# Performance work log

Hardware: AMD Instinct MI355X
Metric: run time of the kernel (lower is better)

The kernel has to match this reference:

```python
import jax, jax.numpy as jnp
import numpy as np

# Fixed Grossberg constants (registered buffers in the torch module)
TAU = 0.8          # time constant
DECAY = 0.15       # passive decay A
B_CAP = 1.0        # excitatory cap B
C_FLOOR = 0.1      # inhibitory floor C
LAT_INHIB = 3.0    # lateral inhibition strength
DIV_SIGMA = 0.3    # divisive normalization sigma
ALPHA = 1.5        # excitatory gating alpha
BETA = 0.75        # inhibitory gating beta

BATCH = 32768
N = 17
T = 128
DT = 0.05


def _dynamics(state, W_pos, W_neg, feasibility, P):
    """Grossberg shunting ODE right-hand side. state: [B,17]."""
    # valences evaluated with environmental perturbation
    val_eval = state[:, 13:17] + P[:, 13:17]                       # [B,4]
    gate_exc = jax.nn.sigmoid(ALPHA * val_eval)                    # [B,4]
    gate_inh = jax.nn.sigmoid(-BETA * val_eval)                    # [B,4]
    ones9 = jnp.ones_like(state[:, :9])
    ones4 = jnp.ones_like(gate_exc)
    # gates expanded over nodes: only action nodes (9:13) gated
    ge_full = jnp.concatenate([ones9, gate_exc, ones4], axis=1)    # [B,17]
    gi_full = jnp.concatenate([ones9, gate_inh, ones4], axis=1)    # [B,17]
    # row-gating of W is equivalent to gating the matvec output
    exc = ge_full * jnp.einsum('bij,bj->bi', W_pos, state)         # [B,17]
    inh = gi_full * jnp.einsum('bij,bj->bi', W_neg, state)         # [B,17]
    E = jax.nn.relu(exc)
    I = jax.nn.relu(inh)
    # environmental drive routed through shunting terms for need nodes
    E_needs = E[:, :9] + jax.nn.relu(P[:, :9])
    I_needs = I[:, :9] + jax.nn.relu(-P[:, :9])
    # feasibility gates action excitation; selective lateral inhibition:
    # each action inhibited by the (divisively normalized) sum of OTHER actions
    acts = state[:, 9:13]
    other_sum = jnp.sum(acts, axis=1, keepdims=True) - acts
    lateral = LAT_INHIB * other_sum / (DIV_SIGMA + other_sum)
    E_acts = E[:, 9:13] * feasibility
    I_acts = I[:, 9:13] + lateral
    E_full = jnp.concatenate([E_needs, E_acts, E[:, 13:17]], axis=1)
    I_full = jnp.concatenate([I_needs, I_acts, I[:, 13:17]], axis=1)
    # direct additive perturbation only on valence nodes
    P_direct = jnp.concatenate([jnp.zeros_like(state[:, :13]), P[:, 13:17]], axis=1)
    return (-DECAY * state + (B_CAP - state) * E_full
            - (C_FLOOR + state) * I_full + P_direct) / TAU


def setup_inputs() -> dict:
    key = jax.random.key(0)
    k0, k1, k2, k3, k4 = jax.random.split(key, 5)
    state0 = jax.random.uniform(k0, (BATCH, N), dtype=jnp.float32)
    W_pos = 0.2 * jax.random.uniform(k1, (BATCH, N, N), dtype=jnp.float32)
    W_neg = 0.2 * jax.random.uniform(k2, (BATCH, N, N), dtype=jnp.float32)
    feasibility = jax.random.uniform(k3, (BATCH, 4), dtype=jnp.float32)
    perturbation = 0.1 * jax.random.normal(k4, (BATCH, N), dtype=jnp.float32)
    t_eval = jnp.arange(T, dtype=jnp.float32) * DT
    return {"state0": state0, "W_pos": W_pos, "W_neg": W_neg,
            "feasibility": feasibility, "perturbation": perturbation,
            "t_eval": t_eval}


def reference(state0, W_pos, W_neg, feasibility, perturbation, t_eval):
    dt = t_eval[1] - t_eval[0]
    n_steps = t_eval.shape[0] - 1  # static

    def step(s, _):
        ds = _dynamics(s, W_pos, W_neg, feasibility, perturbation)
        raw = s + dt * ds
        new = jnp.concatenate([
            jnp.clip(raw[:, 0:9], 0.0, 1.0),     # needs
            jnp.clip(raw[:, 9:13], 0.0, 1.0),    # actions
            jnp.clip(raw[:, 13:17], -1.0, 1.0),  # valences
        ], axis=1)
        return new, new

    _, traj = jax.lax.scan(step, state0, None, length=n_steps)
    return jnp.concatenate([state0[None], traj], axis=0)  # [T, B, 17]
```

## Files before the change

### kernel.cpp

```cpp
#include <hip/hip_runtime.h>
#include <stdint.h>


typedef _Float16 h2 __attribute__((ext_vector_type(2)));
typedef __fp16 h2raw __attribute__((ext_vector_type(2)));
typedef float f4a __attribute__((ext_vector_type(4), aligned(4)));

static constexpr int BATCH = 32768;
static constexpr int NN = 17;
static constexpr int TT = 128;

__device__ __forceinline__ uint32_t pk(float a, float b) {
    h2raw h = __builtin_amdgcn_cvt_pkrtz(a, b);
    return __builtin_bit_cast(uint32_t, h);
}
__device__ __forceinline__ float dot2(uint32_t a, uint32_t b, float c) {
    return __builtin_amdgcn_fdot2(__builtin_bit_cast(h2, a),
                                  __builtin_bit_cast(h2, b), c, false);
}
__device__ __forceinline__ float lo16(uint32_t u) {
    h2 h = __builtin_bit_cast(h2, u); return (float)h.x;
}
__device__ __forceinline__ float hi16(uint32_t u) {
    h2 h = __builtin_bit_cast(h2, u); return (float)h.y;
}
template <int K>
__device__ __forceinline__ uint32_t qswz(uint32_t v) {
    return (uint32_t)__builtin_amdgcn_ds_swizzle((int)v, (K << 5) | 0x1C);
}

__global__ __launch_bounds__(256, 2) void hotco_kernel(
    const float* __restrict__ state0,
    const float* __restrict__ Wpos,
    const float* __restrict__ Wneg,
    const float* __restrict__ feas,
    const float* __restrict__ P,
    const float* __restrict__ t_eval,
    float* __restrict__ out)
{
    const int tid = blockIdx.x * blockDim.x + threadIdx.x;
    const int lane4 = tid & 3;
    const int b = tid >> 2;
    if (b >= BATCH) return;

    const int base = (lane4 == 0) ? 0 : (4 * lane4 + 1);
    const int nrows = (lane4 == 0) ? 5 : 4;

    constexpr int pA[9] = {0, 2, 4, 5, 7, 9, 11, 13, 15};
    constexpr int pB[9] = {1, 3, -1, 6, 8, 10, 12, 14, 16};

    uint32_t w[5][9], wn[5][9];
    {
        const float* wpb = Wpos + (size_t)b * (NN * NN);
        const float* wnb = Wneg + (size_t)b * (NN * NN);
#pragma unroll
        for (int t = 0; t < 5; ++t) {
            if (t < nrows) {
                const float* rp = wpb + (base + t) * NN;
                const float* rn = wnb + (base + t) * NN;
#pragma unroll
                for (int c = 0; c < 9; ++c) {
                    float a2 = (pB[c] < 0) ? 0.f : rp[pB[c]];
                    float b2 = (pB[c] < 0) ? 0.f : rn[pB[c]];
                    w[t][c]  = pk(rp[pA[c]], a2);
                    wn[t][c] = pk(rn[pA[c]], b2);
                }
            } else {
#pragma unroll
                for (int c = 0; c < 9; ++c) { w[t][c] = 0u; wn[t][c] = 0u; }
            }
        }
    }

    float cA[5], cB[5], pdv[4];
#pragma unroll
    for (int t = 0; t < 5; ++t) { cA[t] = 0.f; cB[t] = 0.f; }
#pragma unroll
    for (int t = 0; t < 4; ++t) pdv[t] = 0.f;
    if (lane4 < 2) {
#pragma unroll
        for (int t = 0; t < 5; ++t) {
            if (t < nrows) {
                float pv = P[(size_t)b * NN + base + t];
                cA[t] = fmaxf(pv, 0.f);
                cB[t] = fmaxf(-pv, 0.f);
            }
        }
    } else if (lane4 == 2) {
#pragma unroll
        for (int t = 0; t < 4; ++t) {
            cA[t] = feas[(size_t)b * 4 + t];
            cB[t] = P[(size_t)b * NN + 13 + t];
        }
    } else {
#pragma unroll
        for (int t = 0; t < 4; ++t)
            pdv[t] = P[(size_t)b * NN + 13 + t];
    }

    uint32_t s2[9];
    {
        const float* sb = state0 + (size_t)b * NN;
        float st[17];
#pragma unroll
        for (int j = 0; j < NN; ++j) st[j] = sb[j];
        s2[0] = pk(st[0], st[1]);   s2[1] = pk(st[2], st[3]);
        s2[2] = pk(st[4], 0.f);     s2[3] = pk(st[5], st[6]);
        s2[4] = pk(st[7], st[8]);   s2[5] = pk(st[9], st[10]);
        s2[6] = pk(st[11], st[12]); s2[7] = pk(st[13], st[14]);
        s2[8] = pk(st[15], st[16]);
    }
    float sOwn[5];
#pragma unroll
    for (int t = 0; t < 5; ++t)
        sOwn[t] = (t < nrows) ? state0[(size_t)b * NN + base + t] : 0.f;

    const float lo = (lane4 == 3) ? -1.f : 0.f;
    const float dtv = t_eval[1] - t_eval[0];
    const float k1 = dtv * 1.25f;
    const float C  = -1.0820212806667226f;

    {
        float* op = out + (size_t)b * NN + base;
        f4a v0; v0.x = sOwn[0]; v0.y = sOwn[1]; v0.z = sOwn[2]; v0.w = sOwn[3];
        *(f4a*)op = v0;
        if (nrows == 5) op[4] = sOwn[4];
    }
    float* outp = out + (size_t)BATCH * NN + (size_t)b * NN + base;

#pragma unroll 1
    for (int st = 1; st < TT; ++st) {
        float E5[5], I5[5];
#pragma unroll
        for (int t = 0; t < 5; ++t) {
            float ae = 0.f, ai = 0.f;
#pragma unroll
            for (int c = 0; c < 9; ++c) {
                ae = dot2(w[t][c], s2[c], ae);
                ai = dot2(wn[t][c], s2[c], ai);
            }
            E5[t] = fmaxf(ae, 0.f);
            I5[t] = fmaxf(ai, 0.f);
        }

        if (lane4 == 2) {
            const float sum_acts = sOwn[0] + sOwn[1] + sOwn[2] + sOwn[3];
            const float v13[4] = { lo16(s2[7]), hi16(s2[7]), lo16(s2[8]), hi16(s2[8]) };
#pragma unroll
            for (int t = 0; t < 4; ++t) {
                float v  = v13[t] + cB[t];
                float e1 = __builtin_amdgcn_exp2f(C * v);
                float ge = __builtin_amdgcn_rcpf(fmaf(e1, e1, 1.f));
                float gi = e1 * __builtin_amdgcn_rcpf(1.f + e1);
                E5[t] = ge * E5[t] * cA[t];
                float os  = sum_acts - sOwn[t];
                float lat = fmaf(-0.9f, __builtin_amdgcn_rcpf(0.3f + os), 3.0f);
                I5[t] = fmaf(gi, I5[t], lat);
            }
            E5[4] = 0.f; I5[4] = 0.f;
        } else {
#pragma unroll
            for (int t = 0; t < 5; ++t) { E5[t] += cA[t]; I5[t] += cB[t]; }
        }

#pragma unroll
        for (int t = 0; t < 5; ++t) {
            float s  = sOwn[t];
            float d0 = fmaf(-0.15f, s, (t < 4) ? pdv[t] : 0.f);
            float d1 = fmaf(1.f - s, E5[t], d0);
            float d2 = fmaf(-(0.1f + s), I5[t], d1);
            float raw = fmaf(k1, d2, s);
            sOwn[t] = fminf(fmaxf(raw, lo), 1.f);
        }

        uint32_t p0 = pk(sOwn[0], sOwn[1]);
        uint32_t p1 = pk(sOwn[2], sOwn[3]);
        uint32_t p2 = pk(sOwn[4], 0.f);
        s2[0] = qswz<0>(p0); s2[1] = qswz<0>(p1); s2[2] = qswz<0>(p2);
        s2[3] = qswz<1>(p0); s2[4] = qswz<1>(p1);
        s2[5] = qswz<2>(p0); s2[6] = qswz<2>(p1);
        s2[7] = qswz<3>(p0); s2[8] = qswz<3>(p1);

        {
            f4a v0; v0.x = sOwn[0]; v0.y = sOwn[1]; v0.z = sOwn[2]; v0.w = sOwn[3];
            *(f4a*)outp = v0;
            if (nrows == 5) outp[4] = sOwn[4];
        }
        outp += (size_t)BATCH * NN;
    }
}

extern "C" void kernel_launch(void* const* d_in, const int* in_sizes, int n_in,
                              void* d_out, int out_size, void* d_ws, size_t ws_size,
                              hipStream_t stream) {
    const float* state0 = (const float*)d_in[0];
    const float* Wpos   = (const float*)d_in[1];
    const float* Wneg   = (const float*)d_in[2];
    const float* feasv  = (const float*)d_in[3];
    const float* P      = (const float*)d_in[4];
    const float* t_eval = (const float*)d_in[5];
    float* out = (float*)d_out;

    dim3 grid(BATCH * 4 / 256), block(256);
    hipLaunchKernelGGL(hotco_kernel, grid, block, 0, stream,
                       state0, Wpos, Wneg, feasv, P, t_eval, out);
}
```

Before: 148.7 us.

## Split each batch element across eight lanes instead of four

Each ODE system is now handled by 8 lanes, each owning 2-3 state rows instead of 4-5. This halves the per-lane dot-product chain and register footprint, which allows higher occupancy (launch bounds raised to 4 blocks/CU) and doubles the thread count. The state is re-broadcast each step through 8-lane ds_swizzle broadcasts, and the valence gating work is split across two lanes. In exchange there are more swizzle ops per step and narrower, less coalesced output stores.

New measurement: 168.9 us. +13.6%, slower.

```diff
diff --git a/kernel.cpp b/kernel.cpp
--- a/kernel.cpp
+++ b/kernel.cpp
@@ -4,7 +4,7 @@
 
 typedef _Float16 h2 __attribute__((ext_vector_type(2)));
 typedef __fp16 h2raw __attribute__((ext_vector_type(2)));
-typedef float f4a __attribute__((ext_vector_type(4), aligned(4)));
+typedef float f2a __attribute__((ext_vector_type(2), aligned(4)));
 
 static constexpr int BATCH = 32768;
 static constexpr int NN = 17;
@@ -25,11 +25,11 @@
     h2 h = __builtin_bit_cast(h2, u); return (float)h.y;
 }
 template <int K>
-__device__ __forceinline__ uint32_t qswz(uint32_t v) {
-    return (uint32_t)__builtin_amdgcn_ds_swizzle((int)v, (K << 5) | 0x1C);
-}
-
-__global__ __launch_bounds__(256, 2) void hotco_kernel(
+__device__ __forceinline__ uint32_t obc(uint32_t v) {
+    return (uint32_t)__builtin_amdgcn_ds_swizzle((int)v, (K << 5) | 0x18);
+}
+
+__global__ __launch_bounds__(256, 4) void hotco_kernel(
     const float* __restrict__ state0,
     const float* __restrict__ Wpos,
     const float* __restrict__ Wneg,
@@ -39,25 +39,24 @@
     float* __restrict__ out)
 {
     const int tid = blockIdx.x * blockDim.x + threadIdx.x;
-    const int lane4 = tid & 3;
-    const int b = tid >> 2;
-    if (b >= BATCH) return;
-
-    const int base = (lane4 == 0) ? 0 : (4 * lane4 + 1);
-    const int nrows = (lane4 == 0) ? 5 : 4;
-
-    constexpr int pA[9] = {0, 2, 4, 5, 7, 9, 11, 13, 15};
-    constexpr int pB[9] = {1, 3, -1, 6, 8, 10, 12, 14, 16};
-
-    uint32_t w[5][9], wn[5][9];
+    const int lq = tid & 7;
+    const int b  = tid >> 3;
+
+    const int sbase = (lq == 0) ? 0 : (2 * lq + 1);
+    const int cnt   = (lq == 0) ? 3 : 2;
+
+    constexpr int pA[9] = {0, 2, 3, 5, 7, 9, 11, 13, 15};
+    constexpr int pB[9] = {1, -1, 4, 6, 8, 10, 12, 14, 16};
+
+    uint32_t w[3][9], wn[3][9];
     {
         const float* wpb = Wpos + (size_t)b * (NN * NN);
         const float* wnb = Wneg + (size_t)b * (NN * NN);
 #pragma unroll
-        for (int t = 0; t < 5; ++t) {
-            if (t < nrows) {
-                const float* rp = wpb + (base + t) * NN;
-                const float* rn = wnb + (base + t) * NN;
+        for (int t = 0; t < 3; ++t) {
+            if (t < cnt) {
+                const float* rp = wpb + (sbase + t) * NN;
+                const float* rn = wnb + (sbase + t) * NN;
 #pragma unroll
                 for (int c = 0; c < 9; ++c) {
                     float a2 = (pB[c] < 0) ? 0.f : rp[pB[c]];
@@ -72,67 +71,68 @@
         }
     }
 
-    float cA[5], cB[5], pdv[4];
-#pragma unroll
-    for (int t = 0; t < 5; ++t) { cA[t] = 0.f; cB[t] = 0.f; }
-#pragma unroll
-    for (int t = 0; t < 4; ++t) pdv[t] = 0.f;
-    if (lane4 < 2) {
-#pragma unroll
-        for (int t = 0; t < 5; ++t) {
-            if (t < nrows) {
-                float pv = P[(size_t)b * NN + base + t];
-                cA[t] = fmaxf(pv, 0.f);
-                cB[t] = fmaxf(-pv, 0.f);
-            }
-        }
-    } else if (lane4 == 2) {
-#pragma unroll
-        for (int t = 0; t < 4; ++t) {
-            cA[t] = feas[(size_t)b * 4 + t];
-            cB[t] = P[(size_t)b * NN + 13 + t];
+    float cE[3], cI[3], cP[3], gP[2], gF[2];
+#pragma unroll
+    for (int t = 0; t < 3; ++t) { cE[t] = 0.f; cI[t] = 0.f; cP[t] = 0.f; }
+    gP[0] = gP[1] = 0.f; gF[0] = gF[1] = 1.f;
+    if (lq < 4) {
+#pragma unroll
+        for (int t = 0; t < 3; ++t) {
+            if (t < cnt) {
+                float pv = P[(size_t)b * NN + sbase + t];
+                cE[t] = fmaxf(pv, 0.f);
+                cI[t] = fmaxf(-pv, 0.f);
+            }
+        }
+    } else if (lq < 6) {
+        const int o = (lq == 4) ? 0 : 2;
+#pragma unroll
+        for (int s = 0; s < 2; ++s) {
+            gP[s] = P[(size_t)b * NN + 13 + o + s];
+            gF[s] = feas[(size_t)b * 4 + o + s];
         }
     } else {
-#pragma unroll
-        for (int t = 0; t < 4; ++t)
-            pdv[t] = P[(size_t)b * NN + 13 + t];
+        const int o = (lq == 6) ? 0 : 2;
+#pragma unroll
+        for (int s = 0; s < 2; ++s)
+            cP[s] = P[(size_t)b * NN + 13 + o + s];
     }
 
     uint32_t s2[9];
     {
-        const float* sb = state0 + (size_t)b * NN;
+        const float* sb_ = state0 + (size_t)b * NN;
         float st[17];
 #pragma unroll
-        for (int j = 0; j < NN; ++j) st[j] = sb[j];
-        s2[0] = pk(st[0], st[1]);   s2[1] = pk(st[2], st[3]);
-        s2[2] = pk(st[4], 0.f);     s2[3] = pk(st[5], st[6]);
+        for (int j = 0; j < NN; ++j) st[j] = sb_[j];
+        s2[0] = pk(st[0], st[1]);   s2[1] = pk(st[2], 0.f);
+        s2[2] = pk(st[3], st[4]);   s2[3] = pk(st[5], st[6]);
         s2[4] = pk(st[7], st[8]);   s2[5] = pk(st[9], st[10]);
         s2[6] = pk(st[11], st[12]); s2[7] = pk(st[13], st[14]);
         s2[8] = pk(st[15], st[16]);
     }
-    float sOwn[5];
-#pragma unroll
-    for (int t = 0; t < 5; ++t)
-        sOwn[t] = (t < nrows) ? state0[(size_t)b * NN + base + t] : 0.f;
-
-    const float lo = (lane4 == 3) ? -1.f : 0.f;
+    float sOwn[3];
+#pragma unroll
+    for (int t = 0; t < 3; ++t)
+        sOwn[t] = (t < cnt) ? state0[(size_t)b * NN + sbase + t] : 0.f;
+
+    const float lo = (lq >= 6) ? -1.f : 0.f;
     const float dtv = t_eval[1] - t_eval[0];
     const float k1 = dtv * 1.25f;
     const float C  = -1.0820212806667226f;
 
     {
-        float* op = out + (size_t)b * NN + base;
-        f4a v0; v0.x = sOwn[0]; v0.y = sOwn[1]; v0.z = sOwn[2]; v0.w = sOwn[3];
-        *(f4a*)op = v0;
-        if (nrows == 5) op[4] = sOwn[4];
-    }
-    float* outp = out + (size_t)BATCH * NN + (size_t)b * NN + base;
+        float* op = out + (size_t)b * NN + sbase;
+        f2a v; v.x = sOwn[0]; v.y = sOwn[1];
+        *(f2a*)op = v;
+        if (lq == 0) op[2] = sOwn[2];
+    }
+    float* outp = out + (size_t)BATCH * NN + (size_t)b * NN + sbase;
 
 #pragma unroll 1
     for (int st = 1; st < TT; ++st) {
-        float E5[5], I5[5];
-#pragma unroll
-        for (int t = 0; t < 5; ++t) {
+        float E5[3], I5[3];
+#pragma unroll
+        for (int t = 0; t < 3; ++t) {
             float ae = 0.f, ai = 0.f;
 #pragma unroll
             for (int c = 0; c < 9; ++c) {
@@ -143,48 +143,48 @@
             I5[t] = fmaxf(ai, 0.f);
         }
 
-        if (lane4 == 2) {
-            const float sum_acts = sOwn[0] + sOwn[1] + sOwn[2] + sOwn[3];
-            const float v13[4] = { lo16(s2[7]), hi16(s2[7]), lo16(s2[8]), hi16(s2[8]) };
-#pragma unroll
-            for (int t = 0; t < 4; ++t) {
-                float v  = v13[t] + cB[t];
+#pragma unroll
+        for (int t = 0; t < 3; ++t) { E5[t] += cE[t]; I5[t] += cI[t]; }
+
+        if ((lq & 6) == 4) {
+            const uint32_t uv = (lq == 4) ? s2[7] : s2[8];
+            const uint32_t ua = (lq == 4) ? s2[5] : s2[6];
+            const float sum_acts = (lo16(s2[5]) + hi16(s2[5]))
+                                 + (lo16(s2[6]) + hi16(s2[6]));
+#pragma unroll
+            for (int s = 0; s < 2; ++s) {
+                float v  = ((s == 0) ? lo16(uv) : hi16(uv)) + gP[s];
                 float e1 = __builtin_amdgcn_exp2f(C * v);
                 float ge = __builtin_amdgcn_rcpf(fmaf(e1, e1, 1.f));
                 float gi = e1 * __builtin_amdgcn_rcpf(1.f + e1);
-                E5[t] = ge * E5[t] * cA[t];
-                float os  = sum_acts - sOwn[t];
+                E5[s] = ge * E5[s] * gF[s];
+                float os  = sum_acts - ((s == 0) ? lo16(ua) : hi16(ua));
                 float lat = fmaf(-0.9f, __builtin_amdgcn_rcpf(0.3f + os), 3.0f);
-                I5[t] = fmaf(gi, I5[t], lat);
-            }
-            E5[4] = 0.f; I5[4] = 0.f;
-        } else {
-#pragma unroll
-            for (int t = 0; t < 5; ++t) { E5[t] += cA[t]; I5[t] += cB[t]; }
-        }
-
-#pragma unroll
-        for (int t = 0; t < 5; ++t) {
+                I5[s] = fmaf(gi, I5[s], lat);
+            }
+        }
+
+#pragma unroll
+        for (int t = 0; t < 3; ++t) {
             float s  = sOwn[t];
-            float d0 = fmaf(-0.15f, s, (t < 4) ? pdv[t] : 0.f);
+            float d0 = fmaf(-0.15f, s, cP[t]);
             float d1 = fmaf(1.f - s, E5[t], d0);
             float d2 = fmaf(-(0.1f + s), I5[t], d1);
             float raw = fmaf(k1, d2, s);
             sOwn[t] = fminf(fmaxf(raw, lo), 1.f);
         }
 
-        uint32_t p0 = pk(sOwn[0], sOwn[1]);
-        uint32_t p1 = pk(sOwn[2], sOwn[3]);
-        uint32_t p2 = pk(sOwn[4], 0.f);
-        s2[0] = qswz<0>(p0); s2[1] = qswz<0>(p1); s2[2] = qswz<0>(p2);
-        s2[3] = qswz<1>(p0); s2[4] = qswz<1>(p1);
-        s2[5] = qswz<2>(p0); s2[6] = qswz<2>(p1);
-        s2[7] = qswz<3>(p0); s2[8] = qswz<3>(p1);
+        uint32_t q0 = pk(sOwn[0], sOwn[1]);
+        uint32_t q1 = pk(sOwn[2], 0.f);
+        s2[0] = obc<0>(q0); s2[1] = obc<0>(q1);
+        s2[2] = obc<1>(q0); s2[3] = obc<2>(q0); s2[4] = obc<3>(q0);
+        s2[5] = obc<4>(q0); s2[6] = obc<5>(q0);
+        s2[7] = obc<6>(q0); s2[8] = obc<7>(q0);
 
         {
-            f4a v0; v0.x = sOwn[0]; v0.y = sOwn[1]; v0.z = sOwn[2]; v0.w = sOwn[3];
-            *(f4a*)outp = v0;
-            if (nrows == 5) outp[4] = sOwn[4];
+            f2a v; v.x = sOwn[0]; v.y = sOwn[1];
+            *(f2a*)outp = v;
+            if (lq == 0) outp[2] = sOwn[2];
         }
         outp += (size_t)BATCH * NN;
     }
@@ -201,7 +201,7 @@
     const float* t_eval = (const float*)d_in[5];
     float* out = (float*)d_out;
 
-    dim3 grid(BATCH * 4 / 256), block(256);
+    dim3 grid(BATCH * 8 / 256), block(256);
     hipLaunchKernelGGL(hotco_kernel, grid, block, 0, stream,
                        state0, Wpos, Wneg, feasv, P, t_eval, out);
 }
```
